# Optimization experiments

Hardware: AMD Instinct MI355X
Metric: run time of the kernel (lower is better)

Reference implementation:

```python
import jax, jax.numpy as jnp
import numpy as np

EMBED_DIM = 1024
NUM_HEADS = 16
HEAD_DIM = EMBED_DIM // NUM_HEADS


def setup_inputs() -> dict:
    key = jax.random.key(0)
    ks = jax.random.split(key, 12)
    B, S, E = 2, 2048, EMBED_DIM
    scale = 1.0 / np.sqrt(E)
    inp = {
        "query": jax.random.normal(ks[0], (B, S, E), dtype=jnp.float32),
        "key": jax.random.normal(ks[1], (B, S, E), dtype=jnp.float32),
        "value": jax.random.normal(ks[2], (B, S, E), dtype=jnp.float32),
        "key_padding_mask": jax.random.randint(ks[3], (B, S), 0, 2).astype(bool),
        # Linear params (torch nn.Linear: y = x @ W.T + b)
        "Wq": jax.random.normal(ks[4], (E, E), dtype=jnp.float32) * scale,
        "bq": jnp.zeros((E,), dtype=jnp.float32),
        "Wk": jax.random.normal(ks[5], (E, E), dtype=jnp.float32) * scale,
        "bk": jnp.zeros((E,), dtype=jnp.float32),
        "Wv": jax.random.normal(ks[6], (E, E), dtype=jnp.float32) * scale,
        "bv": jnp.zeros((E,), dtype=jnp.float32),
        "Wo": jax.random.normal(ks[7], (E, E), dtype=jnp.float32) * scale,
        "bo": jnp.zeros((E,), dtype=jnp.float32),
    }
    return inp


def reference(query, key, value, key_padding_mask, Wq, bq, Wk, bk, Wv, bv, Wo, bo):
    B, Sq, E = query.shape
    H, D = NUM_HEADS, HEAD_DIM

    def split_heads(x, W, b):
        y = x @ W.T + b                      # [B, S, E]
        return y.reshape(B, -1, H, D).transpose(0, 2, 1, 3)  # [B, H, S, D]

    q = split_heads(query, Wq, bq)
    k = split_heads(key, Wk, bk)
    v = split_heads(value, Wv, bv)

    scores = jnp.einsum("bhqd,bhkd->bhqk", q, k) / jnp.sqrt(jnp.float32(D))
    scores = jnp.where(key_padding_mask[:, None, None, :], -jnp.inf, scores)
    probs = jax.nn.softmax(scores, axis=-1)  # dropout p=0.0 -> identity
    attn = jnp.einsum("bhqk,bhkd->bhqd", probs, v)
    attn = attn.transpose(0, 2, 1, 3).reshape(B, Sq, E)
    return attn @ Wo.T + bo
```

## Files before the change

### kernel.cpp

```cpp
#include <hip/hip_runtime.h>
#include <hip/hip_bf16.h>

#define BATCH 2
#define SEQ   2048
#define EMBED 1024
#define NHEAD 16
#define HDIM  64

typedef __bf16 bf16x8 __attribute__((ext_vector_type(8)));
typedef __bf16 bf16x4 __attribute__((ext_vector_type(4)));
typedef float  floatx4 __attribute__((ext_vector_type(4)));

__global__ void mask_flags_bits(const void* qptr, const void* mptr,
                                unsigned long long* mb, int* flags,
                                __hip_bfloat16* mones) {
    const unsigned int* w = (const unsigned int*)mptr;
    int all01 = 1, allf = 1;
    for (int i = 0; i < 64; ++i) {
        unsigned int x = w[i];
        if (!(x == 0u || x == 1u)) all01 = 0;
        if (!(x == 0u || x == 0x3F800000u)) allf = 0;
    }
    const int bytemask = (all01 || allf) ? 0 : 1;
    const int i = blockIdx.x * 64 + threadIdx.x;
    int v;
    if (bytemask) v = (((const unsigned char*)mptr)[i] != 0);
    else          v = (((const unsigned int*)mptr)[i] != 0u);
    unsigned long long bal = __ballot(v);
    if (threadIdx.x == 0) mb[blockIdx.x] = bal;
    mones[i] = __float2bfloat16(v ? 0.f : 1.f);
    if (blockIdx.x == 0 && threadIdx.x == 0) {
        const unsigned short* u = (const unsigned short*)qptr;
        int sane = 0;
        for (int k = 0; k < 64; ++k) {
            int e = (u[2 * k] >> 7) & 0xff;
            if (e >= 117 && e <= 137) sane++;
        }
        flags[0] = (sane >= 40) ? 1 : 0;
        flags[1] = bytemask;
    }
}

struct ConvAll { const void* src[7]; void* dst[7]; unsigned n[7]; };

__global__ __launch_bounds__(256) void convert_all(ConvAll a, const int* flags) {
    if (flags[0]) return;
    const int t = blockIdx.y;
    const unsigned n8 = a.n[t] / 8;
    const unsigned stride = gridDim.x * blockDim.x;
    for (unsigned i = blockIdx.x * blockDim.x + threadIdx.x; i < n8; i += stride) {
        const unsigned base = i * 8;
        const float* s = (const float*)a.src[t] + base;
        __hip_bfloat16 tmp[8];
#pragma unroll
        for (int j = 0; j < 8; ++j) tmp[j] = __float2bfloat16(s[j]);
        *(uint4*)((__hip_bfloat16*)a.dst[t] + base) = *(const uint4*)tmp;
    }
}

__device__ __forceinline__ void gload_lds16(const __hip_bfloat16* g, __bf16* l) {
    __builtin_amdgcn_global_load_lds(
        (const __attribute__((address_space(1))) unsigned int*)g,
        (__attribute__((address_space(3))) unsigned int*)l, 16, 0, 0);
}

struct GemmIO {
    const void* Xr; const __hip_bfloat16* Xc;
    const void* Wr; const __hip_bfloat16* Wc;
    const void* br;
    void* Y;
    float osc;
};
struct GemmArgs { GemmIO io[3]; };

__global__ __launch_bounds__(256, 2) void gemm_mfma(
        GemmArgs args, int M, int N, int K, const int* flags,
        const __hip_bfloat16* __restrict__ mones) {
    const GemmIO io = args.io[blockIdx.z];
    const int isbf = flags[0];
    const __hip_bfloat16* Xp = isbf ? (const __hip_bfloat16*)io.Xr : io.Xc;
    const __hip_bfloat16* Wp = isbf ? (const __hip_bfloat16*)io.Wr : io.Wc;
    __shared__ __bf16 Xs[128 * 64];
    __shared__ __bf16 Ws[128 * 64];
    const int lane = threadIdx.x & 63, wv = threadIdx.x >> 6;
    const int wr = wv >> 1, wc = wv & 1;
    const int l = lane & 15, quad = lane >> 4;
    const int row0 = blockIdx.y * 128, col0 = blockIdx.x * 128;

    const int srow = lane >> 3;
    const int schunk = (lane & 7) ^ srow;
    const __hip_bfloat16* xbase = Xp + (size_t)(row0 + srow) * K + schunk * 8;
    const __hip_bfloat16* wbase = Wp + (size_t)(col0 + srow) * K + schunk * 8;

    floatx4 acc[4][4] = {};

    for (int k0 = 0; k0 < K; k0 += 64) {
        __syncthreads();
#pragma unroll
        for (int i = 0; i < 4; ++i) {
            const int instr = wv * 4 + i;
            gload_lds16(xbase + (size_t)instr * 8 * K + k0, &Xs[instr * 512]);
        }
#pragma unroll
        for (int i = 0; i < 4; ++i) {
            const int instr = wv * 4 + i;
            gload_lds16(wbase + (size_t)instr * 8 * K + k0, &Ws[instr * 512]);
        }
        __syncthreads();
#pragma unroll
        for (int kk = 0; kk < 2; ++kk) {
            bf16x8 af[4], bfr[4];
#pragma unroll
            for (int m = 0; m < 4; ++m)
                af[m] = *(const bf16x8*)
                    &Xs[(wr * 64 + m * 16 + l) * 64 + ((kk * 4 + quad) ^ (l & 7)) * 8];
#pragma unroll
            for (int n = 0; n < 4; ++n)
                bfr[n] = *(const bf16x8*)
                    &Ws[(wc * 64 + n * 16 + l) * 64 + ((kk * 4 + quad) ^ (l & 7)) * 8];
#pragma unroll
            for (int m = 0; m < 4; ++m)
#pragma unroll
                for (int n = 0; n < 4; ++n)
                    acc[m][n] = __builtin_amdgcn_mfma_f32_16x16x32_bf16(
                        af[m], bfr[n], acc[m][n], 0, 0, 0);
        }
    }

    if (blockIdx.z == 2) {
#pragma unroll
        for (int m = 0; m < 4; ++m) {
            const int rb = row0 + wr * 64 + m * 16 + quad * 4;
            const int b = rb >> 11, s0 = rb & (SEQ - 1);
            float mf[4];
#pragma unroll
            for (int r = 0; r < 4; ++r)
                mf[r] = __bfloat162float(mones[rb + r]);
#pragma unroll
            for (int n = 0; n < 4; ++n) {
                const int col = col0 + wc * 64 + n * 16 + l;
                const int h = col >> 6, d = col & 63;
                const float bv = isbf
                    ? __bfloat162float(((const __hip_bfloat16*)io.br)[col])
                    : ((const float*)io.br)[col];
                bf16x4 out;
#pragma unroll
                for (int r = 0; r < 4; ++r)
                    out[r] = (__bf16)((acc[m][n][r] + bv) * mf[r]);
                *(bf16x4*)((__hip_bfloat16*)io.Y +
                           ((size_t)((b << 4) + h) * HDIM + d) * SEQ + s0) = out;
            }
        }
    } else {
#pragma unroll
        for (int m = 0; m < 4; ++m) {
#pragma unroll
            for (int n = 0; n < 4; ++n) {
                const int col = col0 + wc * 64 + n * 16 + l;
                const float bv = isbf
                    ? __bfloat162float(((const __hip_bfloat16*)io.br)[col])
                    : ((const float*)io.br)[col];
#pragma unroll
                for (int r = 0; r < 4; ++r) {
                    const int row = row0 + wr * 64 + m * 16 + quad * 4 + r;
                    const float v = (acc[m][n][r] + bv) * io.osc;
                    ((__hip_bfloat16*)io.Y)[(size_t)row * N + col] = __float2bfloat16(v);
                }
            }
        }
    }
}

__global__ __launch_bounds__(256, 2) void gemm_out(
        const __hip_bfloat16* __restrict__ X,
        const void* __restrict__ Wr, const __hip_bfloat16* __restrict__ Wc,
        const void* __restrict__ bias, void* __restrict__ Y,
        const int* flags) {
    const int N = EMBED, K = EMBED;
    const int isbf = flags[0];
    const __hip_bfloat16* Wp = isbf ? (const __hip_bfloat16*)Wr : Wc;
    __shared__ __bf16 Xs[64 * 64];
    __shared__ __bf16 Ws[128 * 64];
    const int lane = threadIdx.x & 63, wv = threadIdx.x >> 6;
    const int wr = wv >> 1, wc = wv & 1;
    const int l = lane & 15, quad = lane >> 4;
    const int row0 = blockIdx.y * 64, col0 = blockIdx.x * 128;

    const int srow = lane >> 3;
    const int schunk = (lane & 7) ^ srow;
    const __hip_bfloat16* xbase = X + (size_t)(row0 + srow) * K + schunk * 8;
    const __hip_bfloat16* wbase = Wp + (size_t)(col0 + srow) * K + schunk * 8;

    floatx4 acc[2][4] = {};

    for (int k0 = 0; k0 < K; k0 += 64) {
        __syncthreads();
#pragma unroll
        for (int i = 0; i < 2; ++i) {
            const int instr = wv * 2 + i;
            gload_lds16(xbase + (size_t)instr * 8 * K + k0, &Xs[instr * 512]);
        }
#pragma unroll
        for (int i = 0; i < 4; ++i) {
            const int instr = wv * 4 + i;
            gload_lds16(wbase + (size_t)instr * 8 * K + k0, &Ws[instr * 512]);
        }
        __syncthreads();
#pragma unroll
        for (int kk = 0; kk < 2; ++kk) {
            bf16x8 af[2], bfr[4];
#pragma unroll
            for (int m = 0; m < 2; ++m)
                af[m] = *(const bf16x8*)
                    &Xs[(wr * 32 + m * 16 + l) * 64 + ((kk * 4 + quad) ^ (l & 7)) * 8];
#pragma unroll
            for (int n = 0; n < 4; ++n)
                bfr[n] = *(const bf16x8*)
                    &Ws[(wc * 64 + n * 16 + l) * 64 + ((kk * 4 + quad) ^ (l & 7)) * 8];
#pragma unroll
            for (int m = 0; m < 2; ++m)
#pragma unroll
                for (int n = 0; n < 4; ++n)
                    acc[m][n] = __builtin_amdgcn_mfma_f32_16x16x32_bf16(
                        af[m], bfr[n], acc[m][n], 0, 0, 0);
        }
    }

#pragma unroll
    for (int m = 0; m < 2; ++m) {
#pragma unroll
        for (int n = 0; n < 4; ++n) {
            const int col = col0 + wc * 64 + n * 16 + l;
            const float bv = isbf
                ? __bfloat162float(((const __hip_bfloat16*)bias)[col])
                : ((const float*)bias)[col];
#pragma unroll
            for (int r = 0; r < 4; ++r) {
                const int row = row0 + wr * 32 + m * 16 + quad * 4 + r;
                const float v = acc[m][n][r] + bv;
                if (isbf)
                    ((__hip_bfloat16*)Y)[(size_t)row * N + col] = __float2bfloat16(v);
                else
                    ((float*)Y)[(size_t)row * N + col] = v;
            }
        }
    }
}

__global__ __launch_bounds__(256) void attn_mfma(
        const __hip_bfloat16* __restrict__ Qb,
        const __hip_bfloat16* __restrict__ Kb,
        const __hip_bfloat16* __restrict__ Vt,
        const __hip_bfloat16* __restrict__ mones,
        __hip_bfloat16* __restrict__ Ao) {
    const int bh = blockIdx.x, b = bh >> 4, h = bh & 15;
    const int q0 = blockIdx.y * 128;
    const int wv = threadIdx.x >> 6, lane = threadIdx.x & 63;
    const int l = lane & 15, quad = lane >> 4;

    __shared__ __bf16 Ks[2][128 * 64];
    __shared__ __bf16 Vs[2][64 * 128];

    bf16x8 aQ[2][2];
#pragma unroll
    for (int g = 0; g < 2; ++g) {
        const int qrow = q0 + wv * 32 + g * 16 + l;
        const __hip_bfloat16* qp =
            Qb + ((size_t)(b * SEQ + qrow)) * EMBED + h * HDIM + quad * 8;
        aQ[g][0] = *(const bf16x8*)qp;
        aQ[g][1] = *(const bf16x8*)(qp + 32);
    }

    floatx4 O[2][4] = {};
    floatx4 Ol[2] = {};
    const int rho = 8 * (l >> 2) + (l & 3);

    const int ksrow = lane >> 3, kpc = lane & 7;
    const int vsrow = lane >> 4, vpc = lane & 15;
    const __hip_bfloat16* mbase = mones + b * SEQ;

    auto stage = [&](int k0, int buf) {
#pragma unroll
        for (int i = 0; i < 4; ++i) {
            const int row = wv * 32 + i * 8 + ksrow;
            const int sc = kpc ^ ((row & 3) | (((row >> 3) & 1) << 2));
            gload_lds16(Kb + ((size_t)(b * SEQ + k0 + row)) * EMBED + h * HDIM +
                            sc * 8,
                        &Ks[buf][(wv * 32 + i * 8) * 64]);
        }
#pragma unroll
        for (int i = 0; i < 4; ++i) {
            const int row = wv * 16 + i * 4 + vsrow;
            const int sc = vpc ^ (row & 15);
            gload_lds16(Vt + ((size_t)(bh * HDIM + row)) * SEQ + k0 + sc * 8,
                        &Vs[buf][(wv * 16 + i * 4) * 128]);
        }
    };

    stage(0, 0);
    const int NT = SEQ / 128;
    for (int t = 0; t < NT; ++t) {
        __syncthreads();
        if (t + 1 < NT) stage((t + 1) * 128, (t + 1) & 1);
        const int buf = t & 1;
        const int k0 = t * 128;

#pragma unroll
        for (int kh2 = 0; kh2 < 2; ++kh2) {
            bf16x8 a0[4], a1[4];
#pragma unroll
            for (int n = 0; n < 4; ++n) {
                const int rr = kh2 * 64 + 32 * (n >> 1) + 4 * (n & 1) + rho;
                const int f = (rr & 3) | (((rr >> 3) & 1) << 2);
                a0[n] = *(const bf16x8*)&Ks[buf][rr * 64 + ((quad) ^ f) * 8];
                a1[n] = *(const bf16x8*)&Ks[buf][rr * 64 + ((quad + 4) ^ f) * 8];
            }
            bf16x8 bv[2][4];
#pragma unroll
            for (int kh = 0; kh < 2; ++kh)
#pragma unroll
                for (int dt = 0; dt < 4; ++dt) {
                    const int c = kh2 * 8 + kh * 4 + quad;
                    bv[kh][dt] = *(const bf16x8*)
                        &Vs[buf][(dt * 16 + l) * 128 + (c ^ l) * 8];
                }
            bf16x8 vm[2];
#pragma unroll
            for (int kh = 0; kh < 2; ++kh)
                vm[kh] = *(const bf16x8*)
                    (mbase + k0 + kh2 * 64 + kh * 32 + quad * 8);

#pragma unroll
            for (int g = 0; g < 2; ++g) {
                floatx4 S[4];
#pragma unroll
                for (int n = 0; n < 4; ++n) {
                    floatx4 c = {};
                    c = __builtin_amdgcn_mfma_f32_16x16x32_bf16(a0[n], aQ[g][0],
                                                                c, 0, 0, 0);
                    c = __builtin_amdgcn_mfma_f32_16x16x32_bf16(a1[n], aQ[g][1],
                                                                c, 0, 0, 0);
                    S[n] = c;
                }
#pragma unroll
                for (int n = 0; n < 4; ++n)
#pragma unroll
                    for (int r = 0; r < 4; ++r) S[n][r] = exp2f(S[n][r]);
#pragma unroll
                for (int kh = 0; kh < 2; ++kh) {
                    bf16x8 ap;
#pragma unroll
                    for (int j = 0; j < 4; ++j) {
                        ap[j]     = (__bf16)S[2 * kh][j];
                        ap[j + 4] = (__bf16)S[2 * kh + 1][j];
                    }
#pragma unroll
                    for (int dt = 0; dt < 4; ++dt)
                        O[g][dt] = __builtin_amdgcn_mfma_f32_16x16x32_bf16(
                            ap, bv[kh][dt], O[g][dt], 0, 0, 0);
                    Ol[g] = __builtin_amdgcn_mfma_f32_16x16x32_bf16(
                        ap, vm[kh], Ol[g], 0, 0, 0);
                }
            }
        }
    }
#pragma unroll
    for (int g = 0; g < 2; ++g)
#pragma unroll
        for (int r = 0; r < 4; ++r) {
            const float lr = Ol[g][r];
            const float inv = (lr > 0.f) ? (1.f / lr) : 0.f;
            const int row = q0 + wv * 32 + g * 16 + quad * 4 + r;
#pragma unroll
            for (int dt = 0; dt < 4; ++dt)
                Ao[((size_t)(b * SEQ + row)) * EMBED + h * HDIM + dt * 16 + l] =
                    __float2bfloat16(O[g][dt][r] * inv);
        }
}

extern "C" void kernel_launch(void* const* d_in, const int* in_sizes, int n_in,
                              void* d_out, int out_size, void* d_ws, size_t ws_size,
                              hipStream_t stream) {
    const void* query = d_in[0];
    const void* key   = d_in[1];
    const void* value = d_in[2];
    const void* mask  = d_in[3];

    char* ws = (char*)d_ws;
    int* flags = (int*)ws;
    unsigned long long* mbits = (unsigned long long*)(ws + 1024);
    __hip_bfloat16* mones = (__hip_bfloat16*)(ws + 2048);
    const size_t TEN = (size_t)BATCH * SEQ * EMBED;
    const size_t WEL = (size_t)EMBED * EMBED;
    char* p = ws + 32768;
    __hip_bfloat16* Qc  = (__hip_bfloat16*)p;  p += TEN * 2;
    __hip_bfloat16* Kc  = (__hip_bfloat16*)p;  p += TEN * 2;
    __hip_bfloat16* Vc  = (__hip_bfloat16*)p;  p += TEN * 2;
    __hip_bfloat16* Wqc = (__hip_bfloat16*)p;  p += WEL * 2;
    __hip_bfloat16* Wkc = (__hip_bfloat16*)p;  p += WEL * 2;
    __hip_bfloat16* Wvc = (__hip_bfloat16*)p;  p += WEL * 2;
    __hip_bfloat16* Woc = (__hip_bfloat16*)p;  p += WEL * 2;
    __hip_bfloat16* Qb  = (__hip_bfloat16*)p;  p += TEN * 2;
    __hip_bfloat16* Kb  = (__hip_bfloat16*)p;  p += TEN * 2;
    __hip_bfloat16* Vt  = (__hip_bfloat16*)p;  p += TEN * 2;
    __hip_bfloat16* Ao  = Qc;

    const int M = BATCH * SEQ;
    const float QSCALE = 0.125f * 1.44269504088896f;

    mask_flags_bits<<<M / 64, 64, 0, stream>>>(query, mask, mbits, flags, mones);

    ConvAll ca;
    ca.src[0] = query;    ca.dst[0] = Qc;  ca.n[0] = (unsigned)TEN;
    ca.src[1] = key;      ca.dst[1] = Kc;  ca.n[1] = (unsigned)TEN;
    ca.src[2] = value;    ca.dst[2] = Vc;  ca.n[2] = (unsigned)TEN;
    ca.src[3] = d_in[4];  ca.dst[3] = Wqc; ca.n[3] = (unsigned)WEL;
    ca.src[4] = d_in[6];  ca.dst[4] = Wkc; ca.n[4] = (unsigned)WEL;
    ca.src[5] = d_in[8];  ca.dst[5] = Wvc; ca.n[5] = (unsigned)WEL;
    ca.src[6] = d_in[10]; ca.dst[6] = Woc; ca.n[6] = (unsigned)WEL;
    convert_all<<<dim3(64, 7), 256, 0, stream>>>(ca, flags);

    GemmArgs qkv;
    qkv.io[0] = { query, Qc, d_in[4],  Wqc, d_in[5],  (void*)Qb, QSCALE };
    qkv.io[1] = { key,   Kc, d_in[6],  Wkc, d_in[7],  (void*)Kb, 1.0f };
    qkv.io[2] = { value, Vc, d_in[8],  Wvc, d_in[9],  (void*)Vt, 1.0f };
    gemm_mfma<<<dim3(EMBED / 128, M / 128, 3), 256, 0, stream>>>(
        qkv, M, EMBED, EMBED, flags, mones);

    attn_mfma<<<dim3(BATCH * NHEAD, SEQ / 128), 256, 0, stream>>>(
        Qb, Kb, Vt, mones, Ao);

    gemm_out<<<dim3(EMBED / 128, M / 64), 256, 0, stream>>>(
        Ao, d_in[10], Woc, d_in[11], d_out, flags);
}
```

Before: 245.1 us.

## Shrink attention tiles to 64 queries and 64 keys per block

The attention kernel now handles 64 query rows per block (16 per wave) instead of 128, and stages 64-key tiles of K and V instead of 128. The grid doubles, register and LDS use per block drop, and launch bounds request 4 blocks per CU, so more waves can be resident to hide latency across the 256 CUs. The cost is that each K/V tile is reused by half as many queries, which doubles global/L2 traffic for K and V and doubles the number of barriers per key.

```diff
diff --git a/kernel.cpp b/kernel.cpp
--- a/kernel.cpp
+++ b/kernel.cpp
@@ -247,135 +247,121 @@
     }
 }
 
-__global__ __launch_bounds__(256) void attn_mfma(
+__global__ __launch_bounds__(256, 4) void attn_mfma(
         const __hip_bfloat16* __restrict__ Qb,
         const __hip_bfloat16* __restrict__ Kb,
         const __hip_bfloat16* __restrict__ Vt,
         const __hip_bfloat16* __restrict__ mones,
         __hip_bfloat16* __restrict__ Ao) {
     const int bh = blockIdx.x, b = bh >> 4, h = bh & 15;
-    const int q0 = blockIdx.y * 128;
+    const int q0 = blockIdx.y * 64;
     const int wv = threadIdx.x >> 6, lane = threadIdx.x & 63;
     const int l = lane & 15, quad = lane >> 4;
 
-    __shared__ __bf16 Ks[2][128 * 64];
-    __shared__ __bf16 Vs[2][64 * 128];
-
-    bf16x8 aQ[2][2];
-#pragma unroll
-    for (int g = 0; g < 2; ++g) {
-        const int qrow = q0 + wv * 32 + g * 16 + l;
+    __shared__ __bf16 Ks[2][64 * 64];
+    __shared__ __bf16 Vs[2][64 * 64];
+
+    bf16x8 aQ[2];
+    {
+        const int qrow = q0 + wv * 16 + l;
         const __hip_bfloat16* qp =
             Qb + ((size_t)(b * SEQ + qrow)) * EMBED + h * HDIM + quad * 8;
-        aQ[g][0] = *(const bf16x8*)qp;
-        aQ[g][1] = *(const bf16x8*)(qp + 32);
-    }
-
-    floatx4 O[2][4] = {};
-    floatx4 Ol[2] = {};
+        aQ[0] = *(const bf16x8*)qp;
+        aQ[1] = *(const bf16x8*)(qp + 32);
+    }
+
+    floatx4 O[4] = {};
+    floatx4 Ol = {};
     const int rho = 8 * (l >> 2) + (l & 3);
 
-    const int ksrow = lane >> 3, kpc = lane & 7;
-    const int vsrow = lane >> 4, vpc = lane & 15;
+    const int srow8 = lane >> 3, pc8 = lane & 7;
     const __hip_bfloat16* mbase = mones + b * SEQ;
 
     auto stage = [&](int k0, int buf) {
 #pragma unroll
-        for (int i = 0; i < 4; ++i) {
-            const int row = wv * 32 + i * 8 + ksrow;
-            const int sc = kpc ^ ((row & 3) | (((row >> 3) & 1) << 2));
+        for (int i = 0; i < 2; ++i) {
+            const int row = wv * 16 + i * 8 + srow8;
+            const int sc = pc8 ^ ((row & 3) | (((row >> 3) & 1) << 2));
             gload_lds16(Kb + ((size_t)(b * SEQ + k0 + row)) * EMBED + h * HDIM +
                             sc * 8,
-                        &Ks[buf][(wv * 32 + i * 8) * 64]);
-        }
-#pragma unroll
-        for (int i = 0; i < 4; ++i) {
-            const int row = wv * 16 + i * 4 + vsrow;
-            const int sc = vpc ^ (row & 15);
+                        &Ks[buf][(wv * 16 + i * 8) * 64]);
+        }
+#pragma unroll
+        for (int i = 0; i < 2; ++i) {
+            const int row = wv * 16 + i * 8 + srow8;
+            const int sc = pc8 ^ (row & 7);
             gload_lds16(Vt + ((size_t)(bh * HDIM + row)) * SEQ + k0 + sc * 8,
-                        &Vs[buf][(wv * 16 + i * 4) * 128]);
+                        &Vs[buf][(wv * 16 + i * 8) * 64]);
         }
     };
 
     stage(0, 0);
-    const int NT = SEQ / 128;
+    const int NT = SEQ / 64;
     for (int t = 0; t < NT; ++t) {
         __syncthreads();
-        if (t + 1 < NT) stage((t + 1) * 128, (t + 1) & 1);
+        if (t + 1 < NT) stage((t + 1) * 64, (t + 1) & 1);
         const int buf = t & 1;
-        const int k0 = t * 128;
-
-#pragma unroll
-        for (int kh2 = 0; kh2 < 2; ++kh2) {
-            bf16x8 a0[4], a1[4];
-#pragma unroll
-            for (int n = 0; n < 4; ++n) {
-                const int rr = kh2 * 64 + 32 * (n >> 1) + 4 * (n & 1) + rho;
-                const int f = (rr & 3) | (((rr >> 3) & 1) << 2);
-                a0[n] = *(const bf16x8*)&Ks[buf][rr * 64 + ((quad) ^ f) * 8];
-                a1[n] = *(const bf16x8*)&Ks[buf][rr * 64 + ((quad + 4) ^ f) * 8];
+        const int k0 = t * 64;
+
+        bf16x8 a0[4], a1[4];
+#pragma unroll
+        for (int n = 0; n < 4; ++n) {
+            const int rr = 32 * (n >> 1) + 4 * (n & 1) + rho;
+            const int f = (rr & 3) | (((rr >> 3) & 1) << 2);
+            a0[n] = *(const bf16x8*)&Ks[buf][rr * 64 + (quad ^ f) * 8];
+            a1[n] = *(const bf16x8*)&Ks[buf][rr * 64 + ((quad + 4) ^ f) * 8];
+        }
+        bf16x8 bv[2][4];
+#pragma unroll
+        for (int kh = 0; kh < 2; ++kh)
+#pragma unroll
+            for (int dt = 0; dt < 4; ++dt) {
+                const int c = kh * 4 + quad;
+                bv[kh][dt] = *(const bf16x8*)
+                    &Vs[buf][(dt * 16 + l) * 64 + (c ^ (l & 7)) * 8];
             }
-            bf16x8 bv[2][4];
-#pragma unroll
-            for (int kh = 0; kh < 2; ++kh)
-#pragma unroll
-                for (int dt = 0; dt < 4; ++dt) {
-                    const int c = kh2 * 8 + kh * 4 + quad;
-                    bv[kh][dt] = *(const bf16x8*)
-                        &Vs[buf][(dt * 16 + l) * 128 + (c ^ l) * 8];
-                }
-            bf16x8 vm[2];
-#pragma unroll
-            for (int kh = 0; kh < 2; ++kh)
-                vm[kh] = *(const bf16x8*)
-                    (mbase + k0 + kh2 * 64 + kh * 32 + quad * 8);
-
-#pragma unroll
-            for (int g = 0; g < 2; ++g) {
-                floatx4 S[4];
-#pragma unroll
-                for (int n = 0; n < 4; ++n) {
-                    floatx4 c = {};
-                    c = __builtin_amdgcn_mfma_f32_16x16x32_bf16(a0[n], aQ[g][0],
-                                                                c, 0, 0, 0);
-                    c = __builtin_amdgcn_mfma_f32_16x16x32_bf16(a1[n], aQ[g][1],
-                                                                c, 0, 0, 0);
-                    S[n] = c;
-                }
-#pragma unroll
-                for (int n = 0; n < 4; ++n)
-#pragma unroll
-                    for (int r = 0; r < 4; ++r) S[n][r] = exp2f(S[n][r]);
-#pragma unroll
-                for (int kh = 0; kh < 2; ++kh) {
-                    bf16x8 ap;
-#pragma unroll
-                    for (int j = 0; j < 4; ++j) {
-                        ap[j]     = (__bf16)S[2 * kh][j];
-                        ap[j + 4] = (__bf16)S[2 * kh + 1][j];
-                    }
-#pragma unroll
-                    for (int dt = 0; dt < 4; ++dt)
-                        O[g][dt] = __builtin_amdgcn_mfma_f32_16x16x32_bf16(
-                            ap, bv[kh][dt], O[g][dt], 0, 0, 0);
-                    Ol[g] = __builtin_amdgcn_mfma_f32_16x16x32_bf16(
-                        ap, vm[kh], Ol[g], 0, 0, 0);
-                }
+        bf16x8 vm[2];
+#pragma unroll
+        for (int kh = 0; kh < 2; ++kh)
+            vm[kh] = *(const bf16x8*)(mbase + k0 + kh * 32 + quad * 8);
+
+        floatx4 S[4];
+#pragma unroll
+        for (int n = 0; n < 4; ++n) {
+            floatx4 c = {};
+            c = __builtin_amdgcn_mfma_f32_16x16x32_bf16(a0[n], aQ[0], c, 0, 0, 0);
+            c = __builtin_amdgcn_mfma_f32_16x16x32_bf16(a1[n], aQ[1], c, 0, 0, 0);
+            S[n] = c;
+        }
+#pragma unroll
+        for (int n = 0; n < 4; ++n)
+#pragma unroll
+            for (int r = 0; r < 4; ++r) S[n][r] = exp2f(S[n][r]);
+#pragma unroll
+        for (int kh = 0; kh < 2; ++kh) {
+            bf16x8 ap;
+#pragma unroll
+            for (int j = 0; j < 4; ++j) {
+                ap[j]     = (__bf16)S[2 * kh][j];
+                ap[j + 4] = (__bf16)S[2 * kh + 1][j];
             }
-        }
-    }
-#pragma unroll
-    for (int g = 0; g < 2; ++g)
-#pragma unroll
-        for (int r = 0; r < 4; ++r) {
-            const float lr = Ol[g][r];
-            const float inv = (lr > 0.f) ? (1.f / lr) : 0.f;
-            const int row = q0 + wv * 32 + g * 16 + quad * 4 + r;
 #pragma unroll
             for (int dt = 0; dt < 4; ++dt)
-                Ao[((size_t)(b * SEQ + row)) * EMBED + h * HDIM + dt * 16 + l] =
-                    __float2bfloat16(O[g][dt][r] * inv);
-        }
+                O[dt] = __builtin_amdgcn_mfma_f32_16x16x32_bf16(
+                    ap, bv[kh][dt], O[dt], 0, 0, 0);
+            Ol = __builtin_amdgcn_mfma_f32_16x16x32_bf16(ap, vm[kh], Ol, 0, 0, 0);
+        }
+    }
+#pragma unroll
+    for (int r = 0; r < 4; ++r) {
+        const float lr = Ol[r];
+        const float inv = (lr > 0.f) ? (1.f / lr) : 0.f;
+        const int row = q0 + wv * 16 + quad * 4 + r;
+#pragma unroll
+        for (int dt = 0; dt < 4; ++dt)
+            Ao[((size_t)(b * SEQ + row)) * EMBED + h * HDIM + dt * 16 + l] =
+                __float2bfloat16(O[dt][r] * inv);
+    }
 }
 
 extern "C" void kernel_launch(void* const* d_in, const int* in_sizes, int n_in,
@@ -427,7 +413,7 @@
     gemm_mfma<<<dim3(EMBED / 128, M / 128, 3), 256, 0, stream>>>(
         qkv, M, EMBED, EMBED, flags, mones);
 
-    attn_mfma<<<dim3(BATCH * NHEAD, SEQ / 128), 256, 0, stream>>>(
+    attn_mfma<<<dim3(BATCH * NHEAD, SEQ / 64), 256, 0, stream>>>(
         Qb, Kb, Vt, mones, Ao);
 
     gemm_out<<<dim3(EMBED / 128, M / 64), 256, 0, stream>>>(
```

After: 245.8 us. About the same (+0.3%).
